# Kernel tuning notes

Hardware: AMD Instinct MI355X
Metric: run time of the kernel (lower is better)

The kernel has to match this reference:

```python
import jax, jax.numpy as jnp
import numpy as np

NUM_HEADS = 8
WEIGHTS_DIM = 512
INPUT_DIM = 512
D_HEAD = WEIGHTS_DIM // NUM_HEADS


def setup_inputs() -> dict:
    key = jax.random.key(0)
    ks = jax.random.split(key, 9)
    B, S, D = 4, 2048, INPUT_DIM
    s_in = 1.0 / np.sqrt(D)
    s_w = 1.0 / np.sqrt(WEIGHTS_DIM)
    return {
        "x": jax.random.normal(ks[0], (B, S, D), dtype=jnp.float32),
        "Wq": jax.random.normal(ks[1], (D, WEIGHTS_DIM), dtype=jnp.float32) * s_in,
        "bq": jnp.zeros((WEIGHTS_DIM,), dtype=jnp.float32),
        "Wk": jax.random.normal(ks[2], (D, WEIGHTS_DIM), dtype=jnp.float32) * s_in,
        "bk": jnp.zeros((WEIGHTS_DIM,), dtype=jnp.float32),
        "Wv": jax.random.normal(ks[3], (D, WEIGHTS_DIM), dtype=jnp.float32) * s_in,
        "bv": jnp.zeros((WEIGHTS_DIM,), dtype=jnp.float32),
        "Wh": jax.random.normal(ks[4], (WEIGHTS_DIM, D), dtype=jnp.float32) * s_w,
        "bh": jnp.zeros((D,), dtype=jnp.float32),
    }


def _split_heads(t):
    # [B, S, Dm] -> [B, H, S, d_head]
    B, S, _ = t.shape
    return t.reshape(B, S, NUM_HEADS, D_HEAD).transpose(0, 2, 1, 3)


def reference(x, Wq, bq, Wk, bk, Wv, bv, Wh, bh):
    q = _split_heads(x @ Wq + bq)
    k = _split_heads(x @ Wk + bk)
    v = _split_heads(x @ Wv + bv)
    scale = 1.0 / jnp.sqrt(jnp.float32(D_HEAD))
    scores = jnp.einsum("bhqd,bhkd->bhqk", q, k) * scale  # [B,H,S,S]
    weights = jax.nn.softmax(scores, axis=-1)
    attn = jnp.einsum("bhqk,bhkd->bhqd", weights, v)
    B, H, S, d = attn.shape
    concat = attn.transpose(0, 2, 1, 3).reshape(B, S, H * d)
    return concat @ Wh + bh
```

## Files before the change

kernel.cpp:

```cpp
#include <hip/hip_runtime.h>
#include <stdint.h>

#define NB  4
#define SS  2048
#define DD  512
#define HH  8
#define DHH 64
#define MM  (NB * SS)

typedef __attribute__((ext_vector_type(8))) short bf16x8;
typedef __attribute__((ext_vector_type(4))) float f32x4;
typedef __attribute__((ext_vector_type(16))) float f32x16;
typedef __attribute__((ext_vector_type(4))) short s16x4;

union fu32 { float f; unsigned u; };
union pfu  { uint4 u; bf16x8 v; };

static __device__ __forceinline__ short f2bf(float f) {
  fu32 a; a.f = f;
  unsigned u = a.u;
  return (short)((u + 0x7fffu + ((u >> 16) & 1u)) >> 16);
}
static __device__ __forceinline__ float bf2f(short s) {
  fu32 t; t.u = ((unsigned)(unsigned short)s) << 16;
  return t.f;
}

static __device__ __forceinline__ unsigned cvt_pk_bf16(float lo, float hi) {
  unsigned r;
  asm("v_cvt_pk_bf16_f32 %0, %1, %2" : "=v"(r) : "v"(lo), "v"(hi));
  return r;
}
static __device__ __forceinline__ void permlane32_swap(unsigned& a, unsigned& b) {
  asm("v_permlane32_swap_b32 %0, %1" : "+v"(a), "+v"(b));
}

static __device__ __forceinline__ void async16(const void* g, void* l) {
  __builtin_amdgcn_global_load_lds(
      (__attribute__((address_space(1))) unsigned*)(void*)g,
      (__attribute__((address_space(3))) unsigned*)l, 16, 0, 0);
}

__global__ __launch_bounds__(256) void prep_kernel(
    const float* __restrict__ x, short* __restrict__ xb,
    const float* __restrict__ W0, const float* __restrict__ W1,
    const float* __restrict__ W2, const float* __restrict__ W3,
    short* __restrict__ T0, short* __restrict__ T1,
    short* __restrict__ T2, short* __restrict__ T3) {
  const int bid = blockIdx.x, tid = threadIdx.x;
  if (bid < 2048) {
    int i = (bid * 256 + tid) * 8;
    float4 v0 = *(const float4*)(x + i);
    float4 v1 = *(const float4*)(x + i + 4);
    bf16x8 o;
    o[0] = f2bf(v0.x); o[1] = f2bf(v0.y); o[2] = f2bf(v0.z); o[3] = f2bf(v0.w);
    o[4] = f2bf(v1.x); o[5] = f2bf(v1.y); o[6] = f2bf(v1.z); o[7] = f2bf(v1.w);
    *(bf16x8*)(xb + i) = o;
  } else {
    int z = bid - 2048;
    int widx = z >> 6, rem = z & 63;
    const float* W = widx == 0 ? W0 : widx == 1 ? W1 : widx == 2 ? W2 : W3;
    short*       T = widx == 0 ? T0 : widx == 1 ? T1 : widx == 2 ? T2 : T3;
    int n  = (rem & 7) * 64 + (tid & 63);
    int k0 = (rem >> 3) * 64 + (tid >> 6) * 16;
    bf16x8 t0, t1;
#pragma unroll
    for (int j = 0; j < 8; ++j) t0[j] = f2bf(W[(size_t)(k0 + j) * DD + n]);
#pragma unroll
    for (int j = 0; j < 8; ++j) t1[j] = f2bf(W[(size_t)(k0 + 8 + j) * DD + n]);
    *(bf16x8*)(T + (size_t)n * DD + k0)     = t0;
    *(bf16x8*)(T + (size_t)n * DD + k0 + 8) = t1;
  }
}

__global__ __launch_bounds__(256, 4) void gemm_qkv_kernel(
    const short* __restrict__ A, const short* __restrict__ Bt,
    const float* __restrict__ bq, const float* __restrict__ bk,
    const float* __restrict__ bv, short* __restrict__ qout,
    short* __restrict__ kout, short* __restrict__ vtout, float qscale) {
  __shared__ __align__(16) short a_sh[64 * 64];
  __shared__ __align__(16) short b_sh[128 * 64];
  const int tid  = threadIdx.x;
  const int w    = tid >> 6, lane = tid & 63, quad = lane >> 4, l16 = lane & 15;
  const int m0   = blockIdx.y * 64, n0 = blockIdx.x * 128;
  const int mw   = (w >> 1) * 32,   nw = (w & 1) * 64;
  const int rw   = lane >> 3, seg = lane & 7, gs = seg ^ rw;
  const int sxz  = l16 & 7;

  f32x4 acc[2][4];
#pragma unroll
  for (int i = 0; i < 2; ++i)
#pragma unroll
    for (int j = 0; j < 4; ++j) acc[i][j] = {0.f, 0.f, 0.f, 0.f};

  for (int kt = 0; kt < DD; kt += 64) {
    __syncthreads();
    {
      const short* ga = A  + (size_t)(m0 + w * 16 + rw) * DD + kt + gs * 8;
      const short* gb = Bt + (size_t)(n0 + w * 32 + rw) * DD + kt + gs * 8;
#pragma unroll
      for (int i = 0; i < 2; ++i)
        async16(ga + (size_t)i * 8 * DD, &a_sh[(w * 16 + i * 8) * 64]);
#pragma unroll
      for (int i = 0; i < 4; ++i)
        async16(gb + (size_t)i * 8 * DD, &b_sh[(w * 32 + i * 8) * 64]);
    }
    __syncthreads();
#pragma unroll
    for (int ks = 0; ks < 2; ++ks) {
      const int so = ((ks * 4 + quad) ^ sxz) * 8;
      bf16x8 af[2], bfr[4];
#pragma unroll
      for (int mt = 0; mt < 2; ++mt)
        af[mt] = *(const bf16x8*)&a_sh[(mw + mt * 16 + l16) * 64 + so];
#pragma unroll
      for (int nt = 0; nt < 4; ++nt)
        bfr[nt] = *(const bf16x8*)&b_sh[(nw + nt * 16 + l16) * 64 + so];
#pragma unroll
      for (int mt = 0; mt < 2; ++mt)
#pragma unroll
        for (int nt = 0; nt < 4; ++nt)
          acc[mt][nt] = __builtin_amdgcn_mfma_f32_16x16x32_bf16(
              af[mt], bfr[nt], acc[mt][nt], 0, 0, 0);
    }
  }

#pragma unroll
  for (int nt = 0; nt < 4; ++nt) {
    const int n   = n0 + nw + nt * 16 + l16;
    const int sg  = n >> 9, n9 = n & 511, h = n9 >> 6, d = n & 63;
    const float bval = (sg == 0 ? bq : sg == 1 ? bk : bv)[n9];
    const float scl  = (sg == 0) ? qscale : 1.0f;
#pragma unroll
    for (int mt = 0; mt < 2; ++mt) {
      const int mb = m0 + mw + mt * 16 + quad * 4;
      const int bi = mb >> 11, s = mb & (SS - 1);
      if (sg == 2) {
        s16x4 pk;
#pragma unroll
        for (int r = 0; r < 4; ++r) pk[r] = f2bf(acc[mt][nt][r] + bval);
        *(s16x4*)&vtout[((size_t)(bi * HH + h) * DHH + d) * SS + s] = pk;
      } else {
        short* o = (sg == 0) ? qout : kout;
        const size_t base = ((size_t)(bi * HH + h) * SS + s) * DHH + d;
#pragma unroll
        for (int r = 0; r < 4; ++r)
          o[base + (size_t)r * DHH] = f2bf((acc[mt][nt][r] + bval) * scl);
      }
    }
  }
}

__global__ __launch_bounds__(256, 4) void attn_kernel(
    const short* __restrict__ Qa, const short* __restrict__ Ka,
    const short* __restrict__ Vt, short* __restrict__ Op0,
    short* __restrict__ Op1, float* __restrict__ lpw) {
  __shared__ __align__(16) short k_sh[2][64 * 64];
  __shared__ __align__(16) short vt_sh[2][64 * 64];

  const int tid  = threadIdx.x;
  const int w    = tid >> 6, lane = tid & 63;
  const int l32  = lane & 31, hl = lane >> 5;
  const int n    = blockIdx.x;
  const int grp  = (n & 7) * 8 + (n >> 7);
  const int qt_b = (n >> 3) & 15;
  const int half = grp & 1, h = (grp >> 1) & 7, b = grp >> 4;
  const int q0   = qt_b * 128;
  const int rw = lane >> 3, seg = lane & 7, gs = seg ^ rw;
  const size_t base = (size_t)(b * HH + h) * SS * DHH;
  const short* Qg = Qa + base + (size_t)(q0 + w * 32) * DHH;
  const short* Kg = Ka + base;
  const short* Vg = Vt + base;

  bf16x8 qf[4];
#pragma unroll
  for (int ds = 0; ds < 4; ++ds)
    qf[ds] = *(const bf16x8*)(Qg + (size_t)l32 * DHH + ds * 16 + hl * 8);

  bf16x8 ones;
#pragma unroll
  for (int j = 0; j < 8; ++j) ones[j] = (short)0x3F80;

  f32x16 o_acc[2];
  f32x16 l_acc;
#pragma unroll
  for (int i = 0; i < 16; ++i) { o_acc[0][i] = 0.f; o_acc[1][i] = 0.f; l_acc[i] = 0.f; }

  const int kstart = half * (SS / 2);
  const int kend   = kstart + SS / 2;

  auto stage = [&](int bsel, int kb) {
    const short* gk = Kg + (size_t)(kb + w * 16 + rw) * DHH + gs * 8;
#pragma unroll
    for (int i = 0; i < 2; ++i)
      async16(gk + (size_t)i * 8 * DHH, &k_sh[bsel][(w * 16 + i * 8) * 64]);
#pragma unroll
    for (int i = 0; i < 2; ++i) {
      const int d = w * 16 + i * 8 + rw;
      async16(Vg + (size_t)d * SS + kb + gs * 8,
              &vt_sh[bsel][(w * 16 + i * 8) * 64]);
    }
  };

  stage(0, kstart);
  __syncthreads();
  int cur = 0;

  for (int kb = kstart; kb < kend; kb += 64) {
    if (kb + 64 < kend) stage(cur ^ 1, kb + 64);

#pragma unroll
    for (int ck = 0; ck < 2; ++ck) {
      const int krow = ck * 32 + l32;
      bf16x8 kf[4];
#pragma unroll
      for (int ds = 0; ds < 4; ++ds) {
        const int sseg = (ds * 2 + hl) ^ (krow & 7);
        kf[ds] = *(const bf16x8*)&k_sh[cur][krow * 64 + sseg * 8];
      }
      f32x16 s;
#pragma unroll
      for (int i = 0; i < 16; ++i) s[i] = 0.f;
#pragma unroll
      for (int ds = 0; ds < 4; ++ds)
        s = __builtin_amdgcn_mfma_f32_32x32x16_bf16(kf[ds], qf[ds], s, 0, 0, 0);

#pragma unroll
      for (int i = 0; i < 16; ++i) s[i] = __builtin_amdgcn_exp2f(s[i]);
      unsigned wpk[8];
#pragma unroll
      for (int i = 0; i < 8; ++i) wpk[i] = cvt_pk_bf16(s[2 * i], s[2 * i + 1]);
      permlane32_swap(wpk[0], wpk[2]);
      permlane32_swap(wpk[1], wpk[3]);
      permlane32_swap(wpk[4], wpk[6]);
      permlane32_swap(wpk[5], wpk[7]);
      pfu a0, a1;
      a0.u.x = wpk[0]; a0.u.y = wpk[1]; a0.u.z = wpk[2]; a0.u.w = wpk[3];
      a1.u.x = wpk[4]; a1.u.y = wpk[5]; a1.u.z = wpk[6]; a1.u.w = wpk[7];

      l_acc = __builtin_amdgcn_mfma_f32_32x32x16_bf16(a0.v, ones, l_acc, 0, 0, 0);
      l_acc = __builtin_amdgcn_mfma_f32_32x32x16_bf16(a1.v, ones, l_acc, 0, 0, 0);

#pragma unroll
      for (int dt = 0; dt < 2; ++dt) {
        const int drow = dt * 32 + l32;
#pragma unroll
        for (int ks = 0; ks < 2; ++ks) {
          const int sseg = (ck * 4 + ks * 2 + hl) ^ (drow & 7);
          bf16x8 vf = *(const bf16x8*)&vt_sh[cur][drow * 64 + sseg * 8];
          o_acc[dt] = __builtin_amdgcn_mfma_f32_32x32x16_bf16(
              ks == 0 ? a0.v : a1.v, vf, o_acc[dt], 0, 0, 0);
        }
      }
    }

    __syncthreads();
    cur ^= 1;
  }

  short* Op = half ? Op1 : Op0;
#pragma unroll
  for (int r = 0; r < 16; ++r) {
    const int qg = q0 + w * 32 + (r & 3) + 8 * (r >> 2) + 4 * hl;
    const size_t row = (size_t)(b * HH + h) * SS + qg;
    if (l32 == 0)
      lpw[(size_t)half * (NB * HH * SS) + row] = l_acc[r];
    const float inv = __builtin_amdgcn_rcpf(l_acc[r]);
#pragma unroll
    for (int dt = 0; dt < 2; ++dt)
      Op[row * DHH + dt * 32 + l32] = f2bf(o_acc[dt][r] * inv);
  }
}

__global__ void attn_combine_kernel(const short* __restrict__ Op0,
                                    const short* __restrict__ Op1,
                                    const float* __restrict__ lpw,
                                    short* __restrict__ aws) {
  int idx  = blockIdx.x * 256 + threadIdx.x;
  int dsg  = idx & 7;
  int row  = idx >> 3;
  int q    = row & (SS - 1);
  int bh   = row >> 11, h = bh & 7, b = bh >> 3;
  float l1 = lpw[row], l2 = lpw[NB * HH * SS + row];
  float inv = 1.f / (l1 + l2);
  float w1 = l1 * inv, w2 = l2 * inv;
  bf16x8 a = *(const bf16x8*)&Op0[(size_t)row * DHH + dsg * 8];
  bf16x8 c = *(const bf16x8*)&Op1[(size_t)row * DHH + dsg * 8];
  bf16x8 o;
#pragma unroll
  for (int j = 0; j < 8; ++j) o[j] = f2bf(w1 * bf2f(a[j]) + w2 * bf2f(c[j]));
  *(bf16x8*)&aws[((size_t)(b * SS + q)) * DD + h * DHH + dsg * 8] = o;
}

__global__ __launch_bounds__(256, 4) void gemm_proj_kernel(
    const short* __restrict__ A, const short* __restrict__ Bt,
    const float* __restrict__ bias, float* __restrict__ out) {
  __shared__ __align__(16) short a_sh[64 * 64];
  __shared__ __align__(16) short b_sh[64 * 64];
  const int tid = threadIdx.x;
  const int w   = tid >> 6, lane = tid & 63, quad = lane >> 4, l16 = lane & 15;
  const int m0  = blockIdx.y * 64, n0 = blockIdx.x * 64;
  const int mw  = (w >> 1) * 32, nw = (w & 1) * 32;
  const int rw  = lane >> 3, seg = lane & 7, gs = seg ^ rw;
  const int sxz = l16 & 7;

  f32x4 acc[2][2];
#pragma unroll
  for (int i = 0; i < 2; ++i)
#pragma unroll
    for (int j = 0; j < 2; ++j) acc[i][j] = {0.f, 0.f, 0.f, 0.f};

  for (int kt = 0; kt < DD; kt += 64) {
    __syncthreads();
    {
      const short* ga = A  + (size_t)(m0 + w * 16 + rw) * DD + kt + gs * 8;
      const short* gb = Bt + (size_t)(n0 + w * 16 + rw) * DD + kt + gs * 8;
#pragma unroll
      for (int i = 0; i < 2; ++i) {
        async16(ga + (size_t)i * 8 * DD, &a_sh[(w * 16 + i * 8) * 64]);
        async16(gb + (size_t)i * 8 * DD, &b_sh[(w * 16 + i * 8) * 64]);
      }
    }
    __syncthreads();
#pragma unroll
    for (int ks = 0; ks < 2; ++ks) {
      const int so = ((ks * 4 + quad) ^ sxz) * 8;
      bf16x8 af0 = *(const bf16x8*)&a_sh[(mw + l16) * 64 + so];
      bf16x8 af1 = *(const bf16x8*)&a_sh[(mw + 16 + l16) * 64 + so];
#pragma unroll
      for (int nt = 0; nt < 2; ++nt) {
        bf16x8 bfr = *(const bf16x8*)&b_sh[(nw + nt * 16 + l16) * 64 + so];
        acc[0][nt] = __builtin_amdgcn_mfma_f32_16x16x32_bf16(af0, bfr, acc[0][nt], 0, 0, 0);
        acc[1][nt] = __builtin_amdgcn_mfma_f32_16x16x32_bf16(af1, bfr, acc[1][nt], 0, 0, 0);
      }
    }
  }

#pragma unroll
  for (int nt = 0; nt < 2; ++nt) {
    const int   n  = n0 + nw + nt * 16 + l16;
    const float bv = bias[n];
#pragma unroll
    for (int mt = 0; mt < 2; ++mt)
#pragma unroll
      for (int r = 0; r < 4; ++r) {
        const int m = m0 + mw + mt * 16 + quad * 4 + r;
        out[(size_t)m * DD + n] = acc[mt][nt][r] + bv;
      }
  }
}

extern "C" void kernel_launch(void* const* d_in, const int* in_sizes, int n_in,
                              void* d_out, int out_size, void* d_ws, size_t ws_size,
                              hipStream_t stream) {
  (void)in_sizes; (void)n_in; (void)out_size; (void)ws_size;
  const float* x  = (const float*)d_in[0];
  const float* Wq = (const float*)d_in[1];
  const float* bq = (const float*)d_in[2];
  const float* Wk = (const float*)d_in[3];
  const float* bk = (const float*)d_in[4];
  const float* Wv = (const float*)d_in[5];
  const float* bv = (const float*)d_in[6];
  const float* Wh = (const float*)d_in[7];
  const float* bh = (const float*)d_in[8];

  short* ws  = (short*)d_ws;
  short* xb  = ws;
  short* wqt = xb  + (size_t)MM * DD;
  short* wkt = wqt + (size_t)DD * DD;
  short* wvt = wkt + (size_t)DD * DD;
  short* wht = wvt + (size_t)DD * DD;
  short* qws = wht + (size_t)DD * DD;
  short* kws = qws + (size_t)MM * DD;
  short* vws = kws + (size_t)MM * DD;
  short* aws = vws + (size_t)MM * DD;
  short* op1 = aws + (size_t)MM * DD;
  float* lpw = (float*)(op1 + (size_t)MM * DD);

  hipLaunchKernelGGL(prep_kernel, dim3(2048 + 256), dim3(256), 0, stream,
                     x, xb, Wq, Wk, Wv, Wh, wqt, wkt, wvt, wht);

  const float qscale = 1.4426950408889634f / 8.0f;
  hipLaunchKernelGGL(gemm_qkv_kernel, dim3(12, 128), dim3(256), 0, stream,
                     xb, wqt, bq, bk, bv, qws, kws, vws, qscale);

  hipLaunchKernelGGL(attn_kernel, dim3(1024), dim3(256), 0, stream,
                     qws, kws, vws, xb, op1, lpw);
  hipLaunchKernelGGL(attn_combine_kernel, dim3(NB * HH * SS * 8 / 256), dim3(256), 0, stream,
                     xb, op1, lpw, aws);

  hipLaunchKernelGGL(gemm_proj_kernel, dim3(8, 128), dim3(256), 0, stream,
                     aws, wht, bh, (float*)d_out);
}
```

Baseline: 164.8 us.

## Process two query tiles per wave in attention to reuse K/V fragments

```diff
diff --git a/kernel.cpp b/kernel.cpp
--- a/kernel.cpp
+++ b/kernel.cpp
@@ -151,7 +151,7 @@
   }
 }
 
-__global__ __launch_bounds__(256, 4) void attn_kernel(
+__global__ __launch_bounds__(256, 2) void attn_kernel(
     const short* __restrict__ Qa, const short* __restrict__ Ka,
     const short* __restrict__ Vt, short* __restrict__ Op0,
     short* __restrict__ Op1, float* __restrict__ lpw) {
@@ -162,29 +162,35 @@
   const int w    = tid >> 6, lane = tid & 63;
   const int l32  = lane & 31, hl = lane >> 5;
   const int n    = blockIdx.x;
-  const int grp  = (n & 7) * 8 + (n >> 7);
-  const int qt_b = (n >> 3) & 15;
+  const int grp  = (n & 7) * 8 + (n >> 6);
+  const int qt_b = (n >> 3) & 7;
   const int half = grp & 1, h = (grp >> 1) & 7, b = grp >> 4;
-  const int q0   = qt_b * 128;
+  const int q0   = qt_b * 256;
   const int rw = lane >> 3, seg = lane & 7, gs = seg ^ rw;
   const size_t base = (size_t)(b * HH + h) * SS * DHH;
-  const short* Qg = Qa + base + (size_t)(q0 + w * 32) * DHH;
+  const short* Qg = Qa + base + (size_t)(q0 + w * 64) * DHH;
   const short* Kg = Ka + base;
   const short* Vg = Vt + base;
 
-  bf16x8 qf[4];
-#pragma unroll
-  for (int ds = 0; ds < 4; ++ds)
-    qf[ds] = *(const bf16x8*)(Qg + (size_t)l32 * DHH + ds * 16 + hl * 8);
+  bf16x8 qf[2][4];
+#pragma unroll
+  for (int qx = 0; qx < 2; ++qx)
+#pragma unroll
+    for (int ds = 0; ds < 4; ++ds)
+      qf[qx][ds] = *(const bf16x8*)(Qg + (size_t)(qx * 32 + l32) * DHH + ds * 16 + hl * 8);
 
   bf16x8 ones;
 #pragma unroll
   for (int j = 0; j < 8; ++j) ones[j] = (short)0x3F80;
 
-  f32x16 o_acc[2];
-  f32x16 l_acc;
-#pragma unroll
-  for (int i = 0; i < 16; ++i) { o_acc[0][i] = 0.f; o_acc[1][i] = 0.f; l_acc[i] = 0.f; }
+  f32x16 o_acc[2][2];
+  f32x16 l_acc[2];
+#pragma unroll
+  for (int i = 0; i < 16; ++i) {
+    o_acc[0][0][i] = 0.f; o_acc[0][1][i] = 0.f;
+    o_acc[1][0][i] = 0.f; o_acc[1][1][i] = 0.f;
+    l_acc[0][i] = 0.f; l_acc[1][i] = 0.f;
+  }
 
   const int kstart = half * (SS / 2);
   const int kend   = kstart + SS / 2;
@@ -218,28 +224,44 @@
         const int sseg = (ds * 2 + hl) ^ (krow & 7);
         kf[ds] = *(const bf16x8*)&k_sh[cur][krow * 64 + sseg * 8];
       }
-      f32x16 s;
-#pragma unroll
-      for (int i = 0; i < 16; ++i) s[i] = 0.f;
-#pragma unroll
-      for (int ds = 0; ds < 4; ++ds)
-        s = __builtin_amdgcn_mfma_f32_32x32x16_bf16(kf[ds], qf[ds], s, 0, 0, 0);
-
-#pragma unroll
-      for (int i = 0; i < 16; ++i) s[i] = __builtin_amdgcn_exp2f(s[i]);
-      unsigned wpk[8];
-#pragma unroll
-      for (int i = 0; i < 8; ++i) wpk[i] = cvt_pk_bf16(s[2 * i], s[2 * i + 1]);
-      permlane32_swap(wpk[0], wpk[2]);
-      permlane32_swap(wpk[1], wpk[3]);
-      permlane32_swap(wpk[4], wpk[6]);
-      permlane32_swap(wpk[5], wpk[7]);
-      pfu a0, a1;
-      a0.u.x = wpk[0]; a0.u.y = wpk[1]; a0.u.z = wpk[2]; a0.u.w = wpk[3];
-      a1.u.x = wpk[4]; a1.u.y = wpk[5]; a1.u.z = wpk[6]; a1.u.w = wpk[7];
-
-      l_acc = __builtin_amdgcn_mfma_f32_32x32x16_bf16(a0.v, ones, l_acc, 0, 0, 0);
-      l_acc = __builtin_amdgcn_mfma_f32_32x32x16_bf16(a1.v, ones, l_acc, 0, 0, 0);
+      f32x16 sarr[2];
+#pragma unroll
+      for (int qx = 0; qx < 2; ++qx) {
+#pragma unroll
+        for (int i = 0; i < 16; ++i) sarr[qx][i] = 0.f;
+      }
+      __builtin_amdgcn_s_setprio(1);
+#pragma unroll
+      for (int ds = 0; ds < 4; ++ds) {
+        sarr[0] = __builtin_amdgcn_mfma_f32_32x32x16_bf16(kf[ds], qf[0][ds], sarr[0], 0, 0, 0);
+        sarr[1] = __builtin_amdgcn_mfma_f32_32x32x16_bf16(kf[ds], qf[1][ds], sarr[1], 0, 0, 0);
+      }
+      __builtin_amdgcn_s_setprio(0);
+
+      pfu a[2][2];
+#pragma unroll
+      for (int qx = 0; qx < 2; ++qx) {
+#pragma unroll
+        for (int i = 0; i < 16; ++i) sarr[qx][i] = __builtin_amdgcn_exp2f(sarr[qx][i]);
+        unsigned wpk[8];
+#pragma unroll
+        for (int i = 0; i < 8; ++i)
+          wpk[i] = cvt_pk_bf16(sarr[qx][2 * i], sarr[qx][2 * i + 1]);
+        permlane32_swap(wpk[0], wpk[2]);
+        permlane32_swap(wpk[1], wpk[3]);
+        permlane32_swap(wpk[4], wpk[6]);
+        permlane32_swap(wpk[5], wpk[7]);
+        a[qx][0].u.x = wpk[0]; a[qx][0].u.y = wpk[1];
+        a[qx][0].u.z = wpk[2]; a[qx][0].u.w = wpk[3];
+        a[qx][1].u.x = wpk[4]; a[qx][1].u.y = wpk[5];
+        a[qx][1].u.z = wpk[6]; a[qx][1].u.w = wpk[7];
+      }
+
+      __builtin_amdgcn_s_setprio(1);
+      l_acc[0] = __builtin_amdgcn_mfma_f32_32x32x16_bf16(a[0][0].v, ones, l_acc[0], 0, 0, 0);
+      l_acc[0] = __builtin_amdgcn_mfma_f32_32x32x16_bf16(a[0][1].v, ones, l_acc[0], 0, 0, 0);
+      l_acc[1] = __builtin_amdgcn_mfma_f32_32x32x16_bf16(a[1][0].v, ones, l_acc[1], 0, 0, 0);
+      l_acc[1] = __builtin_amdgcn_mfma_f32_32x32x16_bf16(a[1][1].v, ones, l_acc[1], 0, 0, 0);
 
 #pragma unroll
       for (int dt = 0; dt < 2; ++dt) {
@@ -248,10 +270,13 @@
         for (int ks = 0; ks < 2; ++ks) {
           const int sseg = (ck * 4 + ks * 2 + hl) ^ (drow & 7);
           bf16x8 vf = *(const bf16x8*)&vt_sh[cur][drow * 64 + sseg * 8];
-          o_acc[dt] = __builtin_amdgcn_mfma_f32_32x32x16_bf16(
-              ks == 0 ? a0.v : a1.v, vf, o_acc[dt], 0, 0, 0);
+          o_acc[0][dt] = __builtin_amdgcn_mfma_f32_32x32x16_bf16(
+              ks == 0 ? a[0][0].v : a[0][1].v, vf, o_acc[0][dt], 0, 0, 0);
+          o_acc[1][dt] = __builtin_amdgcn_mfma_f32_32x32x16_bf16(
+              ks == 0 ? a[1][0].v : a[1][1].v, vf, o_acc[1][dt], 0, 0, 0);
         }
       }
+      __builtin_amdgcn_s_setprio(0);
     }
 
     __syncthreads();
@@ -260,15 +285,18 @@
 
   short* Op = half ? Op1 : Op0;
 #pragma unroll
-  for (int r = 0; r < 16; ++r) {
-    const int qg = q0 + w * 32 + (r & 3) + 8 * (r >> 2) + 4 * hl;
-    const size_t row = (size_t)(b * HH + h) * SS + qg;
-    if (l32 == 0)
-      lpw[(size_t)half * (NB * HH * SS) + row] = l_acc[r];
-    const float inv = __builtin_amdgcn_rcpf(l_acc[r]);
-#pragma unroll
-    for (int dt = 0; dt < 2; ++dt)
-      Op[row * DHH + dt * 32 + l32] = f2bf(o_acc[dt][r] * inv);
+  for (int qx = 0; qx < 2; ++qx) {
+#pragma unroll
+    for (int r = 0; r < 16; ++r) {
+      const int qg = q0 + w * 64 + qx * 32 + (r & 3) + 8 * (r >> 2) + 4 * hl;
+      const size_t row = (size_t)(b * HH + h) * SS + qg;
+      if (l32 == 0)
+        lpw[(size_t)half * (NB * HH * SS) + row] = l_acc[qx][r];
+      const float inv = __builtin_amdgcn_rcpf(l_acc[qx][r]);
+#pragma unroll
+      for (int dt = 0; dt < 2; ++dt)
+        Op[row * DHH + dt * 32 + l32] = f2bf(o_acc[qx][dt][r] * inv);
+    }
   }
 }
 
@@ -384,7 +412,7 @@
   hipLaunchKernelGGL(gemm_qkv_kernel, dim3(12, 128), dim3(256), 0, stream,
                      xb, wqt, bq, bk, bv, qws, kws, vws, qscale);
 
-  hipLaunchKernelGGL(attn_kernel, dim3(1024), dim3(256), 0, stream,
+  hipLaunchKernelGGL(attn_kernel, dim3(512), dim3(256), 0, stream,
                      qws, kws, vws, xb, op1, lpw);
   hipLaunchKernelGGL(attn_combine_kernel, dim3(NB * HH * SS * 8 / 256), dim3(256), 0, stream,
                      xb, op1, lpw, aws);
```

New measurement: 166.3 us. About the same (+0.9%).

## Double-buffer LDS tiles in QKV and projection GEMMs to overlap loads with MFMA

Applied to the files above, without the earlier changes.

```diff
diff --git a/kernel.cpp b/kernel.cpp
--- a/kernel.cpp
+++ b/kernel.cpp
@@ -73,13 +73,13 @@
   }
 }
 
-__global__ __launch_bounds__(256, 4) void gemm_qkv_kernel(
+__global__ __launch_bounds__(256, 3) void gemm_qkv_kernel(
     const short* __restrict__ A, const short* __restrict__ Bt,
     const float* __restrict__ bq, const float* __restrict__ bk,
     const float* __restrict__ bv, short* __restrict__ qout,
     short* __restrict__ kout, short* __restrict__ vtout, float qscale) {
-  __shared__ __align__(16) short a_sh[64 * 64];
-  __shared__ __align__(16) short b_sh[128 * 64];
+  __shared__ __align__(16) short a_sh[2][64 * 64];
+  __shared__ __align__(16) short b_sh[2][128 * 64];
   const int tid  = threadIdx.x;
   const int w    = tid >> 6, lane = tid & 63, quad = lane >> 4, l16 = lane & 15;
   const int m0   = blockIdx.y * 64, n0 = blockIdx.x * 128;
@@ -93,29 +93,33 @@
 #pragma unroll
     for (int j = 0; j < 4; ++j) acc[i][j] = {0.f, 0.f, 0.f, 0.f};
 
+  auto stage = [&](int bsel, int kt) {
+    const short* ga = A  + (size_t)(m0 + w * 16 + rw) * DD + kt + gs * 8;
+    const short* gb = Bt + (size_t)(n0 + w * 32 + rw) * DD + kt + gs * 8;
+#pragma unroll
+    for (int i = 0; i < 2; ++i)
+      async16(ga + (size_t)i * 8 * DD, &a_sh[bsel][(w * 16 + i * 8) * 64]);
+#pragma unroll
+    for (int i = 0; i < 4; ++i)
+      async16(gb + (size_t)i * 8 * DD, &b_sh[bsel][(w * 32 + i * 8) * 64]);
+  };
+
+  stage(0, 0);
+  __syncthreads();
+  int cur = 0;
+
   for (int kt = 0; kt < DD; kt += 64) {
-    __syncthreads();
-    {
-      const short* ga = A  + (size_t)(m0 + w * 16 + rw) * DD + kt + gs * 8;
-      const short* gb = Bt + (size_t)(n0 + w * 32 + rw) * DD + kt + gs * 8;
-#pragma unroll
-      for (int i = 0; i < 2; ++i)
-        async16(ga + (size_t)i * 8 * DD, &a_sh[(w * 16 + i * 8) * 64]);
-#pragma unroll
-      for (int i = 0; i < 4; ++i)
-        async16(gb + (size_t)i * 8 * DD, &b_sh[(w * 32 + i * 8) * 64]);
-    }
-    __syncthreads();
+    if (kt + 64 < DD) stage(cur ^ 1, kt + 64);
 #pragma unroll
     for (int ks = 0; ks < 2; ++ks) {
       const int so = ((ks * 4 + quad) ^ sxz) * 8;
       bf16x8 af[2], bfr[4];
 #pragma unroll
       for (int mt = 0; mt < 2; ++mt)
-        af[mt] = *(const bf16x8*)&a_sh[(mw + mt * 16 + l16) * 64 + so];
+        af[mt] = *(const bf16x8*)&a_sh[cur][(mw + mt * 16 + l16) * 64 + so];
 #pragma unroll
       for (int nt = 0; nt < 4; ++nt)
-        bfr[nt] = *(const bf16x8*)&b_sh[(nw + nt * 16 + l16) * 64 + so];
+        bfr[nt] = *(const bf16x8*)&b_sh[cur][(nw + nt * 16 + l16) * 64 + so];
 #pragma unroll
       for (int mt = 0; mt < 2; ++mt)
 #pragma unroll
@@ -123,6 +127,8 @@
           acc[mt][nt] = __builtin_amdgcn_mfma_f32_16x16x32_bf16(
               af[mt], bfr[nt], acc[mt][nt], 0, 0, 0);
     }
+    __syncthreads();
+    cur ^= 1;
   }
 
 #pragma unroll
@@ -295,8 +301,8 @@
 __global__ __launch_bounds__(256, 4) void gemm_proj_kernel(
     const short* __restrict__ A, const short* __restrict__ Bt,
     const float* __restrict__ bias, float* __restrict__ out) {
-  __shared__ __align__(16) short a_sh[64 * 64];
-  __shared__ __align__(16) short b_sh[64 * 64];
+  __shared__ __align__(16) short a_sh[2][64 * 64];
+  __shared__ __align__(16) short b_sh[2][64 * 64];
   const int tid = threadIdx.x;
   const int w   = tid >> 6, lane = tid & 63, quad = lane >> 4, l16 = lane & 15;
   const int m0  = blockIdx.y * 64, n0 = blockIdx.x * 64;
@@ -310,30 +316,36 @@
 #pragma unroll
     for (int j = 0; j < 2; ++j) acc[i][j] = {0.f, 0.f, 0.f, 0.f};
 
+  auto stage = [&](int bsel, int kt) {
+    const short* ga = A  + (size_t)(m0 + w * 16 + rw) * DD + kt + gs * 8;
+    const short* gb = Bt + (size_t)(n0 + w * 16 + rw) * DD + kt + gs * 8;
+#pragma unroll
+    for (int i = 0; i < 2; ++i) {
+      async16(ga + (size_t)i * 8 * DD, &a_sh[bsel][(w * 16 + i * 8) * 64]);
+      async16(gb + (size_t)i * 8 * DD, &b_sh[bsel][(w * 16 + i * 8) * 64]);
+    }
+  };
+
+  stage(0, 0);
+  __syncthreads();
+  int cur = 0;
+
   for (int kt = 0; kt < DD; kt += 64) {
-    __syncthreads();
-    {
-      const short* ga = A  + (size_t)(m0 + w * 16 + rw) * DD + kt + gs * 8;
-      const short* gb = Bt + (size_t)(n0 + w * 16 + rw) * DD + kt + gs * 8;
-#pragma unroll
-      for (int i = 0; i < 2; ++i) {
-        async16(ga + (size_t)i * 8 * DD, &a_sh[(w * 16 + i * 8) * 64]);
-        async16(gb + (size_t)i * 8 * DD, &b_sh[(w * 16 + i * 8) * 64]);
-      }
-    }
-    __syncthreads();
+    if (kt + 64 < DD) stage(cur ^ 1, kt + 64);
 #pragma unroll
     for (int ks = 0; ks < 2; ++ks) {
       const int so = ((ks * 4 + quad) ^ sxz) * 8;
-      bf16x8 af0 = *(const bf16x8*)&a_sh[(mw + l16) * 64 + so];
-      bf16x8 af1 = *(const bf16x8*)&a_sh[(mw + 16 + l16) * 64 + so];
+      bf16x8 af0 = *(const bf16x8*)&a_sh[cur][(mw + l16) * 64 + so];
+      bf16x8 af1 = *(const bf16x8*)&a_sh[cur][(mw + 16 + l16) * 64 + so];
 #pragma unroll
       for (int nt = 0; nt < 2; ++nt) {
-        bf16x8 bfr = *(const bf16x8*)&b_sh[(nw + nt * 16 + l16) * 64 + so];
+        bf16x8 bfr = *(const bf16x8*)&b_sh[cur][(nw + nt * 16 + l16) * 64 + so];
         acc[0][nt] = __builtin_amdgcn_mfma_f32_16x16x32_bf16(af0, bfr, acc[0][nt], 0, 0, 0);
         acc[1][nt] = __builtin_amdgcn_mfma_f32_16x16x32_bf16(af1, bfr, acc[1][nt], 0, 0, 0);
       }
     }
+    __syncthreads();
+    cur ^= 1;
   }
 
 #pragma unroll
```

New measurement: 174.7 us. +6.1%, slower.
